# Optimization experiments

Measured on AMD Instinct MI355X. Metric: run time of the kernel, lower is better.

## Reference

```python
import jax, jax.numpy as jnp
import numpy as np

N_NODES = 40000
N_EDGES = 640000
N_GRAPHS = 64
D = 128


def setup_inputs() -> dict:
    key = jax.random.key(0)
    ks = jax.random.split(key, 8)
    x = jax.random.normal(ks[0], (N_NODES, D), dtype=jnp.float32)
    edge_index = jax.random.randint(ks[1], (2, N_EDGES), 0, N_NODES, dtype=jnp.int64)
    batch = jnp.sort(jax.random.randint(ks[2], (N_NODES,), 0, N_GRAPHS, dtype=jnp.int64))
    s = 1.0 / np.sqrt(D)
    W_rel1 = jax.random.normal(ks[3], (D, D), dtype=jnp.float32) * s
    W_root1 = jax.random.normal(ks[4], (D, D), dtype=jnp.float32) * s
    W_rel2 = jax.random.normal(ks[5], (D, D), dtype=jnp.float32) * s
    W_root2 = jax.random.normal(ks[6], (D, D), dtype=jnp.float32) * s
    Wc = jax.random.normal(ks[7], (D, D), dtype=jnp.float32) * s
    b1 = jnp.zeros((D,), jnp.float32)
    b2 = jnp.zeros((D,), jnp.float32)
    bc = jnp.zeros((D,), jnp.float32)
    return dict(x=x, edge_index=edge_index, batch=batch,
                W_rel1=W_rel1, W_root1=W_root1, b1=b1,
                W_rel2=W_rel2, W_root2=W_root2, b2=b2,
                Wc=Wc, bc=bc)


def _graph_conv(x, src, dst, W_rel, W_root, b):
    # PyG GraphConv with mean aggregation:
    # out_i = W_rel @ mean_{j in N(i)} x_j + W_root @ x_i + b
    n = x.shape[0]
    msg = x[src]                                              # [E, D] gather
    agg = jax.ops.segment_sum(msg, dst, num_segments=n)       # [N, D]
    deg = jax.ops.segment_sum(jnp.ones_like(dst, dtype=x.dtype), dst, num_segments=n)
    agg = agg / jnp.maximum(deg, 1.0)[:, None]                # mean, 0 if isolated
    return agg @ W_rel.T + x @ W_root.T + b


def reference(x, edge_index, batch, W_rel1, W_root1, b1, W_rel2, W_root2, b2, Wc, bc):
    src, dst = edge_index[0], edge_index[1]
    h = jax.nn.relu(_graph_conv(x, src, dst, W_rel1, W_root1, b1))
    h = jax.nn.relu(_graph_conv(h, src, dst, W_rel2, W_root2, b2))
    # global_mean_pool (dropout is identity in eval mode)
    sums = jax.ops.segment_sum(h, batch, num_segments=N_GRAPHS)          # [G, D]
    cnts = jax.ops.segment_sum(jnp.ones_like(batch, dtype=h.dtype), batch, num_segments=N_GRAPHS)
    pooled = sums / jnp.maximum(cnts, 1.0)[:, None]
    return pooled @ Wc.T + bc
```

## Files before the change

kernel.cpp:

```cpp
#include <hip/hip_runtime.h>

#define DD 128
#define ANODE 4
#define SLOT 128

typedef __attribute__((ext_vector_type(8))) short short8v;
typedef __attribute__((ext_vector_type(4))) float float4v;

static __device__ __forceinline__ unsigned short f2bf(float f) {
  unsigned int u = __float_as_uint(f);
  u = (u + 0x7fffu + ((u >> 16) & 1u)) >> 16;
  return (unsigned short)u;
}
static __device__ __forceinline__ float bf2f(unsigned short h) {
  return __uint_as_float(((unsigned int)h) << 16);
}
static __device__ __forceinline__ float blo(unsigned int u) {
  return __uint_as_float(u << 16);
}
static __device__ __forceinline__ float bhi(unsigned int u) {
  return __uint_as_float(u & 0xffff0000u);
}
static __device__ __forceinline__ unsigned int pk(float lo, float hi) {
  return (unsigned int)f2bf(lo) | ((unsigned int)f2bf(hi) << 16);
}

__global__ void prep_kernel(int* __restrict__ cnt, float* __restrict__ sums,
                            int ncnt, int nsums,
                            const float* __restrict__ Wr1, const float* __restrict__ Wo1,
                            const float* __restrict__ Wr2, const float* __restrict__ Wo2,
                            unsigned short* __restrict__ Bpk,
                            const float* __restrict__ x, unsigned short* __restrict__ XH,
                            unsigned short* __restrict__ XL, int N, int has_lo) {
  int i = blockIdx.x * blockDim.x + threadIdx.x;
  if (i < ncnt) cnt[i] = 0;
  if (i < nsums) sums[i] = 0.f;
  if (i < 8192) {
    int L = i >> 12, rest = i & 4095;
    int kt = rest >> 9, nt = (rest >> 6) & 7, lane = rest & 63;
    int d = nt * 16 + (lane & 15);
    int kbase = kt * 32 + (lane >> 4) * 8;
    const float* Wrel = L ? Wr2 : Wr1;
    const float* Wroot = L ? Wo2 : Wo1;
    unsigned short* o = Bpk + (size_t)i * 8;
    #pragma unroll
    for (int j = 0; j < 8; ++j) {
      int k = kbase + j;
      float w = (k < DD) ? Wrel[d * DD + k] : Wroot[d * DD + (k - DD)];
      o[j] = f2bf(w);
    }
  }
  if (i < N * 32) {
    float4 v = reinterpret_cast<const float4*>(x)[i];
    ushort4 h;
    h.x = f2bf(v.x); h.y = f2bf(v.y); h.z = f2bf(v.z); h.w = f2bf(v.w);
    reinterpret_cast<ushort4*>(XH)[i] = h;
    if (has_lo) {
      ushort4 l;
      l.x = f2bf(v.x - bf2f(h.x)); l.y = f2bf(v.y - bf2f(h.y));
      l.z = f2bf(v.z - bf2f(h.z)); l.w = f2bf(v.w - bf2f(h.w));
      reinterpret_cast<ushort4*>(XL)[i] = l;
    }
  }
}

__global__ void fill_slot(const int* __restrict__ src, const int* __restrict__ dst,
                          int* __restrict__ cnt, unsigned short* __restrict__ slot, int E) {
  int e = blockIdx.x * blockDim.x + threadIdx.x;
  if (e < E) {
    int d = dst[e];
    int p = atomicAdd(&cnt[d], 1);
    if (p < SLOT) slot[(size_t)d * SLOT + p] = (unsigned short)src[e];
  }
}

__global__ __launch_bounds__(256) void gather3(
    const uint4* __restrict__ X4, const unsigned short* __restrict__ slot,
    const int* __restrict__ cnt,
    uint4* __restrict__ AH4, uint4* __restrict__ AL4,
    int N, int has_lo) {
  int node = blockIdx.x * ANODE + (threadIdx.x >> 6);
  if (node >= N) return;
  int lane = threadIdx.x & 63;
  int sub = lane >> 4;
  int sl = lane & 15;
  int dg = cnt[node];
  if (dg > SLOT) dg = SLOT;
  int p = (int)((size_t)0) ;
  int p0 = 0;
  const unsigned short* csr = slot + (size_t)node * SLOT;
  int pe = dg;
  float a0 = 0.f, a1 = 0.f, a2 = 0.f, a3 = 0.f, a4 = 0.f, a5 = 0.f, a6 = 0.f, a7 = 0.f;
  p = p0;
  for (; p + 8 <= pe; p += 8) {
    int s0 = csr[p + sub];
    int s1 = csr[p + 4 + sub];
    uint4 u0 = X4[(size_t)s0 * 16 + sl];
    uint4 u1 = X4[(size_t)s1 * 16 + sl];
    a0 += blo(u0.x) + blo(u1.x);  a1 += bhi(u0.x) + bhi(u1.x);
    a2 += blo(u0.y) + blo(u1.y);  a3 += bhi(u0.y) + bhi(u1.y);
    a4 += blo(u0.z) + blo(u1.z);  a5 += bhi(u0.z) + bhi(u1.z);
    a6 += blo(u0.w) + blo(u1.w);  a7 += bhi(u0.w) + bhi(u1.w);
  }
  for (; p < pe; p += 4) {
    int q = p + sub;
    bool act = q < pe;
    int s0 = act ? (int)csr[q] : 0;
    uint4 u0 = X4[(size_t)s0 * 16 + sl];
    if (act) {
      a0 += blo(u0.x); a1 += bhi(u0.x);
      a2 += blo(u0.y); a3 += bhi(u0.y);
      a4 += blo(u0.z); a5 += bhi(u0.z);
      a6 += blo(u0.w); a7 += bhi(u0.w);
    }
  }
  #define RED2(v) v += __shfl_xor(v, 16, 64); v += __shfl_xor(v, 32, 64);
  RED2(a0) RED2(a1) RED2(a2) RED2(a3) RED2(a4) RED2(a5) RED2(a6) RED2(a7)
  #undef RED2
  float inv = 1.f / fmaxf((float)dg, 1.f);
  a0 *= inv; a1 *= inv; a2 *= inv; a3 *= inv;
  a4 *= inv; a5 *= inv; a6 *= inv; a7 *= inv;
  if (sub == 0) {
    uint4 h;
    h.x = pk(a0, a1); h.y = pk(a2, a3); h.z = pk(a4, a5); h.w = pk(a6, a7);
    AH4[(size_t)node * 16 + sl] = h;
    if (has_lo) {
      uint4 l;
      l.x = pk(a0 - bf2f((unsigned short)(h.x & 0xffff)), a1 - bf2f((unsigned short)(h.x >> 16)));
      l.y = pk(a2 - bf2f((unsigned short)(h.y & 0xffff)), a3 - bf2f((unsigned short)(h.y >> 16)));
      l.z = pk(a4 - bf2f((unsigned short)(h.z & 0xffff)), a5 - bf2f((unsigned short)(h.z >> 16)));
      l.w = pk(a6 - bf2f((unsigned short)(h.w & 0xffff)), a7 - bf2f((unsigned short)(h.w >> 16)));
      AL4[(size_t)node * 16 + sl] = l;
    }
  }
}

__global__ __launch_bounds__(256) void gemm2(
    const unsigned short* __restrict__ AH, const unsigned short* __restrict__ AL,
    const unsigned short* __restrict__ XH, const unsigned short* __restrict__ XL,
    const unsigned short* __restrict__ Bpk, const float* __restrict__ bias,
    unsigned short* __restrict__ HH, unsigned short* __restrict__ HL,
    float* __restrict__ sums, const int* __restrict__ batch,
    int N, int has_lo) {
  int lane = threadIdx.x & 63;
  int wid = threadIdx.x >> 6;
  int m0 = (blockIdx.x * 4 + wid) * 16;
  if (m0 >= N) return;
  int arow = m0 + (lane & 15);
  if (arow >= N) arow = N - 1;
  int koff = (lane >> 4) * 8;
  const short8v* Bf = (const short8v*)Bpk;
  float4v acc[8];
  #pragma unroll
  for (int nt = 0; nt < 8; ++nt) acc[nt] = (float4v){0.f, 0.f, 0.f, 0.f};

  #pragma unroll
  for (int kt = 0; kt < 8; ++kt) {
    const unsigned short* hb = (kt < 4)
        ? (AH + (size_t)arow * DD + kt * 32 + koff)
        : (XH + (size_t)arow * DD + (kt - 4) * 32 + koff);
    short8v ahi = *reinterpret_cast<const short8v*>(hb);
    if (has_lo) {
      const unsigned short* lb = (kt < 4)
          ? (AL + (size_t)arow * DD + kt * 32 + koff)
          : (XL + (size_t)arow * DD + (kt - 4) * 32 + koff);
      short8v alo = *reinterpret_cast<const short8v*>(lb);
      #pragma unroll
      for (int nt = 0; nt < 8; ++nt) {
        short8v b = Bf[(kt * 8 + nt) * 64 + lane];
        acc[nt] = __builtin_amdgcn_mfma_f32_16x16x32_bf16(ahi, b, acc[nt], 0, 0, 0);
        acc[nt] = __builtin_amdgcn_mfma_f32_16x16x32_bf16(alo, b, acc[nt], 0, 0, 0);
      }
    } else {
      #pragma unroll
      for (int nt = 0; nt < 8; ++nt) {
        short8v b = Bf[(kt * 8 + nt) * 64 + lane];
        acc[nt] = __builtin_amdgcn_mfma_f32_16x16x32_bf16(ahi, b, acc[nt], 0, 0, 0);
      }
    }
  }

  int col0 = lane & 15;
  int rbase = m0 + (lane >> 4) * 4;
  if (sums) {
    int gl = batch[m0];
    int me = (m0 + 15 < N) ? m0 + 15 : N - 1;
    int gh = batch[me];
    bool fast = (gl == gh) && (m0 + 16 <= N);
    #pragma unroll
    for (int nt = 0; nt < 8; ++nt) {
      int col = nt * 16 + col0;
      float bv = bias[col];
      float v0 = fmaxf(acc[nt][0] + bv, 0.f);
      float v1 = fmaxf(acc[nt][1] + bv, 0.f);
      float v2 = fmaxf(acc[nt][2] + bv, 0.f);
      float v3 = fmaxf(acc[nt][3] + bv, 0.f);
      if (fast) {
        float s = (v0 + v1) + (v2 + v3);
        s += __shfl_xor(s, 16, 64);
        s += __shfl_xor(s, 32, 64);
        if (lane < 16) atomicAdd(&sums[gl * DD + col], s);
      } else {
        float vv[4] = {v0, v1, v2, v3};
        #pragma unroll
        for (int r = 0; r < 4; ++r) {
          int row = rbase + r;
          if (row < N) atomicAdd(&sums[batch[row] * DD + col], vv[r]);
        }
      }
    }
  } else {
    #pragma unroll
    for (int nt = 0; nt < 8; ++nt) {
      int col = nt * 16 + col0;
      float bv = bias[col];
      #pragma unroll
      for (int r = 0; r < 4; ++r) {
        int row = rbase + r;
        if (row < N) {
          float v = fmaxf(acc[nt][r] + bv, 0.f);
          unsigned short h = f2bf(v);
          HH[(size_t)row * DD + col] = h;
          if (has_lo) HL[(size_t)row * DD + col] = f2bf(v - bf2f(h));
        }
      }
    }
  }
}

__global__ void final_kernel(const float* __restrict__ sums, const int* __restrict__ batch,
                             const float* __restrict__ Wc, const float* __restrict__ bc,
                             float* __restrict__ out, int N, int G) {
  int g = blockIdx.x;
  int d = threadIdx.x;
  __shared__ float p[DD];
  __shared__ float invs;
  if (d == 0) {
    int lo = 0, hi = N;
    while (lo < hi) { int m = (lo + hi) >> 1; if (batch[m] < g) lo = m + 1; else hi = m; }
    int a = lo;
    lo = 0; hi = N;
    while (lo < hi) { int m = (lo + hi) >> 1; if (batch[m] < g + 1) lo = m + 1; else hi = m; }
    invs = 1.0f / fmaxf((float)(lo - a), 1.0f);
  }
  __syncthreads();
  p[d] = sums[g * DD + d] * invs;
  __syncthreads();
  float acc = bc[d];
  #pragma unroll 8
  for (int k = 0; k < DD; ++k) acc += p[k] * Wc[d * DD + k];
  out[g * DD + d] = acc;
}

extern "C" void kernel_launch(void* const* d_in, const int* in_sizes, int n_in,
                              void* d_out, int out_size, void* d_ws, size_t ws_size,
                              hipStream_t stream) {
  const float* x   = (const float*)d_in[0];
  const int*   ei  = (const int*)d_in[1];
  const int* batch = (const int*)d_in[2];
  const float* Wr1 = (const float*)d_in[3];
  const float* Wo1 = (const float*)d_in[4];
  const float* b1  = (const float*)d_in[5];
  const float* Wr2 = (const float*)d_in[6];
  const float* Wo2 = (const float*)d_in[7];
  const float* b2  = (const float*)d_in[8];
  const float* Wc  = (const float*)d_in[9];
  const float* bc  = (const float*)d_in[10];
  float* out = (float*)d_out;

  const int N = in_sizes[0] / DD;
  const int E = in_sizes[1] / 2;
  const int G = out_size / DD;
  const int* src = ei;
  const int* dst = ei + E;

  const int Npad = (N + 64) & ~63;
  int* iws    = (int*)d_ws;
  int* cnt    = iws;
  unsigned short* slot = (unsigned short*)(cnt + Npad);
  float* sums = (float*)(slot + (size_t)N * SLOT);
  unsigned short* Bpk = (unsigned short*)(sums + (size_t)G * DD);

  unsigned short* actbase = Bpk + 65536;
  size_t fixed = (size_t)((char*)actbase - (char*)d_ws);
  size_t arr = (size_t)N * DD * sizeof(unsigned short);
  int has_lo = (ws_size >= fixed + 4 * arr) ? 1 : 0;

  unsigned short* XH = actbase;
  unsigned short* HH = XH + (size_t)N * DD;
  unsigned short* XL = has_lo ? HH + (size_t)N * DD : nullptr;
  unsigned short* HL = has_lo ? XL + (size_t)N * DD : nullptr;

  const int blk = 256;
  prep_kernel<<<(N * 32 + blk - 1) / blk, blk, 0, stream>>>(
      cnt, sums, Npad, G * DD, Wr1, Wo1, Wr2, Wo2, Bpk, x, XH, XL, N, has_lo);
  fill_slot<<<(E + blk - 1) / blk, blk, 0, stream>>>(src, dst, cnt, slot, E);

  int agg_blocks = (N + ANODE - 1) / ANODE;
  int gemm_blocks = (N + 63) / 64;

  unsigned short* AH;
  unsigned short* AL;
  if (has_lo && ws_size >= fixed + 6 * arr) {
    AH = HL + (size_t)N * DD;
    AL = AH + (size_t)N * DD;
  } else {
    has_lo = 0;
    XL = AL = HL = nullptr;
    AH = HH + (size_t)N * DD;
  }

  gather3<<<agg_blocks, 256, 0, stream>>>((const uint4*)XH, slot, cnt,
                                          (uint4*)AH, (uint4*)AL, N, has_lo);
  gemm2<<<gemm_blocks, 256, 0, stream>>>(AH, AL, XH, XL, Bpk, b1,
                                         HH, HL, nullptr, nullptr, N, has_lo);
  gather3<<<agg_blocks, 256, 0, stream>>>((const uint4*)HH, slot, cnt,
                                          (uint4*)AH, (uint4*)AL, N, has_lo);
  gemm2<<<gemm_blocks, 256, 0, stream>>>(AH, AL, HH, HL, Bpk + 32768, b2,
                                         nullptr, nullptr, sums, batch, N, has_lo);

  final_kernel<<<G, DD, 0, stream>>>(sums, batch, Wc, bc, out, N, G);
}
```

Before: 152.3 us.

## Drop low-bf16 split for aggregated features, tile GEMM to 32 rows per wave

The gather no longer writes a low-bf16 residual array for the mean-aggregated features. The GEMM uses only the high part for the neighbour term and keeps the hi/lo split only for the root term. The GEMM becomes one wave per block handling 32 rows with two accumulator sets, so each B fragment load is reused across two MFMAs. fill_slot processes two edges per thread with int2 loads. This cuts memory traffic and MFMA count, at the cost of lower precision on the aggregated term and fewer waves per block in the GEMM.

```diff
diff --git a/kernel.cpp b/kernel.cpp
--- a/kernel.cpp
+++ b/kernel.cpp
@@ -66,8 +66,15 @@
 
 __global__ void fill_slot(const int* __restrict__ src, const int* __restrict__ dst,
                           int* __restrict__ cnt, unsigned short* __restrict__ slot, int E) {
-  int e = blockIdx.x * blockDim.x + threadIdx.x;
-  if (e < E) {
+  int e = (blockIdx.x * blockDim.x + threadIdx.x) * 2;
+  if (e + 1 < E) {
+    int2 s2 = *reinterpret_cast<const int2*>(src + e);
+    int2 d2 = *reinterpret_cast<const int2*>(dst + e);
+    int p0 = atomicAdd(&cnt[d2.x], 1);
+    if (p0 < SLOT) slot[(size_t)d2.x * SLOT + p0] = (unsigned short)s2.x;
+    int p1 = atomicAdd(&cnt[d2.y], 1);
+    if (p1 < SLOT) slot[(size_t)d2.y * SLOT + p1] = (unsigned short)s2.y;
+  } else if (e < E) {
     int d = dst[e];
     int p = atomicAdd(&cnt[d], 1);
     if (p < SLOT) slot[(size_t)d * SLOT + p] = (unsigned short)src[e];
@@ -77,8 +84,7 @@
 __global__ __launch_bounds__(256) void gather3(
     const uint4* __restrict__ X4, const unsigned short* __restrict__ slot,
     const int* __restrict__ cnt,
-    uint4* __restrict__ AH4, uint4* __restrict__ AL4,
-    int N, int has_lo) {
+    uint4* __restrict__ AH4, int N) {
   int node = blockIdx.x * ANODE + (threadIdx.x >> 6);
   if (node >= N) return;
   int lane = threadIdx.x & 63;
@@ -86,12 +92,10 @@
   int sl = lane & 15;
   int dg = cnt[node];
   if (dg > SLOT) dg = SLOT;
-  int p = (int)((size_t)0) ;
-  int p0 = 0;
   const unsigned short* csr = slot + (size_t)node * SLOT;
   int pe = dg;
   float a0 = 0.f, a1 = 0.f, a2 = 0.f, a3 = 0.f, a4 = 0.f, a5 = 0.f, a6 = 0.f, a7 = 0.f;
-  p = p0;
+  int p = 0;
   for (; p + 8 <= pe; p += 8) {
     int s0 = csr[p + sub];
     int s1 = csr[p + 4 + sub];
@@ -124,88 +128,97 @@
     uint4 h;
     h.x = pk(a0, a1); h.y = pk(a2, a3); h.z = pk(a4, a5); h.w = pk(a6, a7);
     AH4[(size_t)node * 16 + sl] = h;
-    if (has_lo) {
-      uint4 l;
-      l.x = pk(a0 - bf2f((unsigned short)(h.x & 0xffff)), a1 - bf2f((unsigned short)(h.x >> 16)));
-      l.y = pk(a2 - bf2f((unsigned short)(h.y & 0xffff)), a3 - bf2f((unsigned short)(h.y >> 16)));
-      l.z = pk(a4 - bf2f((unsigned short)(h.z & 0xffff)), a5 - bf2f((unsigned short)(h.z >> 16)));
-      l.w = pk(a6 - bf2f((unsigned short)(h.w & 0xffff)), a7 - bf2f((unsigned short)(h.w >> 16)));
-      AL4[(size_t)node * 16 + sl] = l;
-    }
-  }
-}
-
-__global__ __launch_bounds__(256) void gemm2(
-    const unsigned short* __restrict__ AH, const unsigned short* __restrict__ AL,
+  }
+}
+
+__global__ __launch_bounds__(64) void gemm3(
+    const unsigned short* __restrict__ AH,
     const unsigned short* __restrict__ XH, const unsigned short* __restrict__ XL,
     const unsigned short* __restrict__ Bpk, const float* __restrict__ bias,
     unsigned short* __restrict__ HH, unsigned short* __restrict__ HL,
     float* __restrict__ sums, const int* __restrict__ batch,
     int N, int has_lo) {
-  int lane = threadIdx.x & 63;
-  int wid = threadIdx.x >> 6;
-  int m0 = (blockIdx.x * 4 + wid) * 16;
+  int lane = threadIdx.x;
+  int m0 = blockIdx.x * 32;
   if (m0 >= N) return;
-  int arow = m0 + (lane & 15);
-  if (arow >= N) arow = N - 1;
+  int r0 = m0 + (lane & 15);
+  int r1 = r0 + 16;
+  if (r0 >= N) r0 = N - 1;
+  if (r1 >= N) r1 = N - 1;
   int koff = (lane >> 4) * 8;
   const short8v* Bf = (const short8v*)Bpk;
-  float4v acc[8];
+  float4v acc0[8], acc1[8];
   #pragma unroll
-  for (int nt = 0; nt < 8; ++nt) acc[nt] = (float4v){0.f, 0.f, 0.f, 0.f};
+  for (int nt = 0; nt < 8; ++nt) {
+    acc0[nt] = (float4v){0.f, 0.f, 0.f, 0.f};
+    acc1[nt] = (float4v){0.f, 0.f, 0.f, 0.f};
+  }
 
   #pragma unroll
   for (int kt = 0; kt < 8; ++kt) {
-    const unsigned short* hb = (kt < 4)
-        ? (AH + (size_t)arow * DD + kt * 32 + koff)
-        : (XH + (size_t)arow * DD + (kt - 4) * 32 + koff);
-    short8v ahi = *reinterpret_cast<const short8v*>(hb);
-    if (has_lo) {
-      const unsigned short* lb = (kt < 4)
-          ? (AL + (size_t)arow * DD + kt * 32 + koff)
-          : (XL + (size_t)arow * DD + (kt - 4) * 32 + koff);
-      short8v alo = *reinterpret_cast<const short8v*>(lb);
+    if (kt < 4) {
+      short8v a0 = *reinterpret_cast<const short8v*>(AH + (size_t)r0 * DD + kt * 32 + koff);
+      short8v a1 = *reinterpret_cast<const short8v*>(AH + (size_t)r1 * DD + kt * 32 + koff);
       #pragma unroll
       for (int nt = 0; nt < 8; ++nt) {
         short8v b = Bf[(kt * 8 + nt) * 64 + lane];
-        acc[nt] = __builtin_amdgcn_mfma_f32_16x16x32_bf16(ahi, b, acc[nt], 0, 0, 0);
-        acc[nt] = __builtin_amdgcn_mfma_f32_16x16x32_bf16(alo, b, acc[nt], 0, 0, 0);
+        acc0[nt] = __builtin_amdgcn_mfma_f32_16x16x32_bf16(a0, b, acc0[nt], 0, 0, 0);
+        acc1[nt] = __builtin_amdgcn_mfma_f32_16x16x32_bf16(a1, b, acc1[nt], 0, 0, 0);
       }
     } else {
-      #pragma unroll
-      for (int nt = 0; nt < 8; ++nt) {
-        short8v b = Bf[(kt * 8 + nt) * 64 + lane];
-        acc[nt] = __builtin_amdgcn_mfma_f32_16x16x32_bf16(ahi, b, acc[nt], 0, 0, 0);
+      int o = (kt - 4) * 32 + koff;
+      short8v x0h = *reinterpret_cast<const short8v*>(XH + (size_t)r0 * DD + o);
+      short8v x1h = *reinterpret_cast<const short8v*>(XH + (size_t)r1 * DD + o);
+      if (has_lo) {
+        short8v x0l = *reinterpret_cast<const short8v*>(XL + (size_t)r0 * DD + o);
+        short8v x1l = *reinterpret_cast<const short8v*>(XL + (size_t)r1 * DD + o);
+        #pragma unroll
+        for (int nt = 0; nt < 8; ++nt) {
+          short8v b = Bf[(kt * 8 + nt) * 64 + lane];
+          acc0[nt] = __builtin_amdgcn_mfma_f32_16x16x32_bf16(x0h, b, acc0[nt], 0, 0, 0);
+          acc0[nt] = __builtin_amdgcn_mfma_f32_16x16x32_bf16(x0l, b, acc0[nt], 0, 0, 0);
+          acc1[nt] = __builtin_amdgcn_mfma_f32_16x16x32_bf16(x1h, b, acc1[nt], 0, 0, 0);
+          acc1[nt] = __builtin_amdgcn_mfma_f32_16x16x32_bf16(x1l, b, acc1[nt], 0, 0, 0);
+        }
+      } else {
+        #pragma unroll
+        for (int nt = 0; nt < 8; ++nt) {
+          short8v b = Bf[(kt * 8 + nt) * 64 + lane];
+          acc0[nt] = __builtin_amdgcn_mfma_f32_16x16x32_bf16(x0h, b, acc0[nt], 0, 0, 0);
+          acc1[nt] = __builtin_amdgcn_mfma_f32_16x16x32_bf16(x1h, b, acc1[nt], 0, 0, 0);
+        }
       }
     }
   }
 
   int col0 = lane & 15;
-  int rbase = m0 + (lane >> 4) * 4;
+  int q = lane >> 4;
   if (sums) {
     int gl = batch[m0];
-    int me = (m0 + 15 < N) ? m0 + 15 : N - 1;
+    int me = (m0 + 31 < N) ? m0 + 31 : N - 1;
     int gh = batch[me];
-    bool fast = (gl == gh) && (m0 + 16 <= N);
+    bool fast = (gl == gh) && (m0 + 32 <= N);
     #pragma unroll
     for (int nt = 0; nt < 8; ++nt) {
       int col = nt * 16 + col0;
       float bv = bias[col];
-      float v0 = fmaxf(acc[nt][0] + bv, 0.f);
-      float v1 = fmaxf(acc[nt][1] + bv, 0.f);
-      float v2 = fmaxf(acc[nt][2] + bv, 0.f);
-      float v3 = fmaxf(acc[nt][3] + bv, 0.f);
       if (fast) {
-        float s = (v0 + v1) + (v2 + v3);
+        float s = 0.f;
+        #pragma unroll
+        for (int r = 0; r < 4; ++r) {
+          s += fmaxf(acc0[nt][r] + bv, 0.f);
+          s += fmaxf(acc1[nt][r] + bv, 0.f);
+        }
         s += __shfl_xor(s, 16, 64);
         s += __shfl_xor(s, 32, 64);
         if (lane < 16) atomicAdd(&sums[gl * DD + col], s);
       } else {
-        float vv[4] = {v0, v1, v2, v3};
         #pragma unroll
         for (int r = 0; r < 4; ++r) {
-          int row = rbase + r;
-          if (row < N) atomicAdd(&sums[batch[row] * DD + col], vv[r]);
+          int row0 = m0 + q * 4 + r;
+          int row1 = row0 + 16;
+          if (row0 < N) atomicAdd(&sums[batch[row0] * DD + col], fmaxf(acc0[nt][r] + bv, 0.f));
+          if (row1 < N) atomicAdd(&sums[batch[row1] * DD + col], fmaxf(acc1[nt][r] + bv, 0.f));
         }
       }
     }
@@ -216,12 +229,19 @@
       float bv = bias[col];
       #pragma unroll
       for (int r = 0; r < 4; ++r) {
-        int row = rbase + r;
-        if (row < N) {
-          float v = fmaxf(acc[nt][r] + bv, 0.f);
+        int row0 = m0 + q * 4 + r;
+        int row1 = row0 + 16;
+        if (row0 < N) {
+          float v = fmaxf(acc0[nt][r] + bv, 0.f);
           unsigned short h = f2bf(v);
-          HH[(size_t)row * DD + col] = h;
-          if (has_lo) HL[(size_t)row * DD + col] = f2bf(v - bf2f(h));
+          HH[(size_t)row0 * DD + col] = h;
+          if (has_lo) HL[(size_t)row0 * DD + col] = f2bf(v - bf2f(h));
+        }
+        if (row1 < N) {
+          float v = fmaxf(acc1[nt][r] + bv, 0.f);
+          unsigned short h = f2bf(v);
+          HH[(size_t)row1 * DD + col] = h;
+          if (has_lo) HL[(size_t)row1 * DD + col] = f2bf(v - bf2f(h));
         }
       }
     }
@@ -284,40 +304,29 @@
   unsigned short* actbase = Bpk + 65536;
   size_t fixed = (size_t)((char*)actbase - (char*)d_ws);
   size_t arr = (size_t)N * DD * sizeof(unsigned short);
-  int has_lo = (ws_size >= fixed + 4 * arr) ? 1 : 0;
+  int has_lo = (ws_size >= fixed + 5 * arr) ? 1 : 0;
 
   unsigned short* XH = actbase;
   unsigned short* HH = XH + (size_t)N * DD;
-  unsigned short* XL = has_lo ? HH + (size_t)N * DD : nullptr;
+  unsigned short* AH = HH + (size_t)N * DD;
+  unsigned short* XL = has_lo ? AH + (size_t)N * DD : nullptr;
   unsigned short* HL = has_lo ? XL + (size_t)N * DD : nullptr;
 
   const int blk = 256;
   prep_kernel<<<(N * 32 + blk - 1) / blk, blk, 0, stream>>>(
       cnt, sums, Npad, G * DD, Wr1, Wo1, Wr2, Wo2, Bpk, x, XH, XL, N, has_lo);
-  fill_slot<<<(E + blk - 1) / blk, blk, 0, stream>>>(src, dst, cnt, slot, E);
+  int half = (E + 1) / 2;
+  fill_slot<<<(half + blk - 1) / blk, blk, 0, stream>>>(src, dst, cnt, slot, E);
 
   int agg_blocks = (N + ANODE - 1) / ANODE;
-  int gemm_blocks = (N + 63) / 64;
-
-  unsigned short* AH;
-  unsigned short* AL;
-  if (has_lo && ws_size >= fixed + 6 * arr) {
-    AH = HL + (size_t)N * DD;
-    AL = AH + (size_t)N * DD;
-  } else {
-    has_lo = 0;
-    XL = AL = HL = nullptr;
-    AH = HH + (size_t)N * DD;
-  }
-
-  gather3<<<agg_blocks, 256, 0, stream>>>((const uint4*)XH, slot, cnt,
-                                          (uint4*)AH, (uint4*)AL, N, has_lo);
-  gemm2<<<gemm_blocks, 256, 0, stream>>>(AH, AL, XH, XL, Bpk, b1,
-                                         HH, HL, nullptr, nullptr, N, has_lo);
-  gather3<<<agg_blocks, 256, 0, stream>>>((const uint4*)HH, slot, cnt,
-                                          (uint4*)AH, (uint4*)AL, N, has_lo);
-  gemm2<<<gemm_blocks, 256, 0, stream>>>(AH, AL, HH, HL, Bpk + 32768, b2,
-                                         nullptr, nullptr, sums, batch, N, has_lo);
+  int gemm_blocks = (N + 31) / 32;
+
+  gather3<<<agg_blocks, 256, 0, stream>>>((const uint4*)XH, slot, cnt, (uint4*)AH, N);
+  gemm3<<<gemm_blocks, 64, 0, stream>>>(AH, XH, XL, Bpk, b1,
+                                        HH, HL, nullptr, nullptr, N, has_lo);
+  gather3<<<agg_blocks, 256, 0, stream>>>((const uint4*)HH, slot, cnt, (uint4*)AH, N);
+  gemm3<<<gemm_blocks, 64, 0, stream>>>(AH, HH, HL, Bpk + 32768, b2,
+                                        nullptr, nullptr, sums, batch, N, has_lo);
 
   final_kernel<<<G, DD, 0, stream>>>(sums, batch, Wc, bc, out, N, G);
 }
```

Result: slower. 182.7 us (+20.0%).
